# Kernel tuning notes

Hardware: AMD Instinct MI355X
Metric: run time of the kernel (lower is better)

## Reference

```python
import jax, jax.numpy as jnp
import numpy as np

ALPHA = 1.702
LIMIT = 7.0


def setup_inputs() -> dict:
    E, H, D = 16, 2880, 2880
    B, S = 2, 1024
    T = B * S
    key = jax.random.key(0)
    ks = jax.random.split(key, 8)
    hidden_states = jax.random.normal(ks[0], (B, S, H), dtype=jnp.float32)
    routing_weights = jax.random.uniform(ks[1], (T, E), dtype=jnp.float32)
    scale = 0.02
    Wg = jax.random.normal(ks[2], (E, H, D), dtype=jnp.float32) * scale
    bg = jax.random.normal(ks[3], (E, D), dtype=jnp.float32) * scale
    Wu = jax.random.normal(ks[4], (E, H, D), dtype=jnp.float32) * scale
    bu = jax.random.normal(ks[5], (E, D), dtype=jnp.float32) * scale
    Wd = jax.random.normal(ks[6], (E, D, H), dtype=jnp.float32) * scale
    bd = jax.random.normal(ks[7], (E, H), dtype=jnp.float32) * scale
    return {"hidden_states": hidden_states, "routing_weights": routing_weights,
            "Wg": Wg, "bg": bg, "Wu": Wu, "bu": bu, "Wd": Wd, "bd": bd}


def reference(hidden_states, routing_weights, Wg, bg, Wu, bu, Wd, bd):
    orig_shape = hidden_states.shape
    H = Wg.shape[1]
    x = hidden_states.reshape(-1, H)  # [T, H]
    # per-expert gate/up projections: [E, T, D]
    gate = jnp.einsum('th,ehd->etd', x, Wg) + bg[:, None, :]
    gate = jnp.minimum(gate, LIMIT)
    up = jnp.einsum('th,ehd->etd', x, Wu) + bu[:, None, :]
    up = jnp.clip(up, -LIMIT, LIMIT)
    glu = gate * jax.nn.sigmoid(gate * ALPHA)
    inter = (up + 1.0) * glu  # [E, T, D]
    # down projection: [E, T, H]
    down = jnp.einsum('etd,edh->eth', inter, Wd) + bd[:, None, :]
    # routing-weighted sum over experts: [T, H]
    out = jnp.einsum('eth,te->th', down, routing_weights)
    return out.reshape(orig_shape)
```

## Files before the change

### kernel.cpp

```cpp
#include <hip/hip_runtime.h>
#include <cstdint>


#define ALPHA 1.702f
#define LIMIT 7.0f

static constexpr int E = 16;
static constexpr int H = 2880;
static constexpr int D = 2880;
static constexpr int T = 2048;
static constexpr int NKT = 45;
static constexpr int NG  = 4;
static constexpr int DP  = 3072;
static constexpr int NPR = 2*DP;

typedef float        f32x4  __attribute__((ext_vector_type(4)));
typedef short        bf16x8 __attribute__((ext_vector_type(8)));

#define MFMA_BF16(a,b,c) __builtin_amdgcn_mfma_f32_16x16x32_bf16((a),(b),(c),0,0,0)
#define SBAR()        __builtin_amdgcn_s_barrier()
#define SCHED_FENCE() __builtin_amdgcn_sched_barrier(0)
#define PRIO1()       __builtin_amdgcn_s_setprio(1)
#define PRIO0()       __builtin_amdgcn_s_setprio(0)
#define LGK0()        asm volatile("s_waitcnt lgkmcnt(0)" ::: "memory")
#define VMC6()        asm volatile("s_waitcnt vmcnt(6)" ::: "memory")

__device__ __forceinline__ unsigned short f2bf(float f){
  unsigned u = __builtin_bit_cast(unsigned, f);
  u += 0x7fffu + ((u >> 16) & 1u);
  return (unsigned short)(u >> 16);
}
__device__ __forceinline__ unsigned pack2(float a, float b){
  return (unsigned)f2bf(a) | ((unsigned)f2bf(b) << 16);
}

__device__ __forceinline__ void gload_lds16(const void* g, void* l){
  __builtin_amdgcn_global_load_lds((const __attribute__((address_space(1))) unsigned*)g,
                                   (__attribute__((address_space(3))) unsigned*)l,
                                   16, 0, 0);
}

__global__ void cvt_kernel(const float* __restrict__ in, unsigned short* __restrict__ ob, int n8){
  int i = blockIdx.x * 256 + threadIdx.x;
  if (i < n8){
    float4 a = ((const float4*)in)[2*i];
    float4 b = ((const float4*)in)[2*i+1];
    uint4 o;
    o.x = pack2(a.x, a.y); o.y = pack2(a.z, a.w);
    o.z = pack2(b.x, b.y); o.w = pack2(b.z, b.w);
    ((uint4*)ob)[i] = o;
  }
}

__global__ __launch_bounds__(256) void tcvt_kernel(
    const float* __restrict__ src, unsigned short* __restrict__ dst,
    int mode, size_t dstStride)
{
  __shared__ unsigned short tl[64*72];
  const int t = threadIdx.x;
  const float* s = src + (size_t)blockIdx.z * H * D;
  unsigned short* o = dst + (size_t)blockIdx.z * dstStride;
  const int r0 = blockIdx.x * 64, c0 = blockIdx.y * 64;

  if (c0 < D){
    int rr = t >> 2;
    #pragma unroll
    for (int p = 0; p < 4; ++p){
      int cc = ((t & 3) + p*4) * 4;
      float4 v = *(const float4*)(s + (size_t)(r0 + rr)*D + c0 + cc);
      tl[(cc+0)*72 + rr] = f2bf(v.x);
      tl[(cc+1)*72 + rr] = f2bf(v.y);
      tl[(cc+2)*72 + rr] = f2bf(v.z);
      tl[(cc+3)*72 + rr] = f2bf(v.w);
    }
    __syncthreads();
    #pragma unroll
    for (int p = 0; p < 2; ++p){
      int task = p*256 + t;
      int cl = task >> 3, ch = task & 7;
      int c = c0 + cl;
      int rowp = (mode < 2) ? ((c >> 5)*64 + (c & 31) + mode*32) : c;
      bf16x8 v = *(const bf16x8*)&tl[cl*72 + ch*8];
      *(bf16x8*)(o + (size_t)rowp*H + r0 + ch*8) = v;
    }
  } else {
    #pragma unroll
    for (int p = 0; p < 2; ++p){
      int task = p*256 + t;
      int cl = task >> 3, ch = task & 7;
      int c = c0 + cl;
      int rowp = (c >> 5)*64 + (c & 31) + mode*32;
      bf16x8 z = (bf16x8){0,0,0,0,0,0,0,0};
      *(bf16x8*)(o + (size_t)rowp*H + r0 + ch*8) = z;
    }
  }
}

__global__ void reduce_kernel(const float* __restrict__ p, float* __restrict__ out, int n4){
  int i = blockIdx.x * 256 + threadIdx.x;
  if (i < n4){
    f32x4 a = ((const f32x4*)p)[i];
    #pragma unroll
    for (int g = 1; g < NG; ++g)
      a += ((const f32x4*)(p + (size_t)g * T * H))[i];
    ((f32x4*)out)[i] = a;
  }
}

__global__ __launch_bounds__(512, 2) void gateup_kernel(
    const unsigned short* __restrict__ xb,
    const unsigned short* __restrict__ wGU,
    const float* __restrict__ bg,
    const float* __restrict__ bu,
    unsigned short* __restrict__ inter,
    int e0)
{
  __shared__ short As[2][256*64];
  __shared__ short Bs[2][256*64];

  const int t = threadIdx.x, lane = t & 63, wv = t >> 6;
  const int wm = wv >> 2, wn = wv & 3;

  int nbx = gridDim.x, nby = gridDim.y;
  int lin = blockIdx.x + nbx*(blockIdx.y + nby*blockIdx.z);
  int per = (nbx*nby*gridDim.z) >> 3;
  int id2 = (lin & 7)*per + (lin >> 3);
  int bx = id2 % nbx; int rem = id2 / nbx;
  int by = rem % nby; int ez = rem / nby;

  const int trow0 = bx*256, ncol0 = by*256;
  const int e = e0 + ez;
  const unsigned short* wg = wGU + (size_t)ez * NPR * H;

  f32x4 acc[8][4];
  #pragma unroll
  for (int i = 0; i < 8; ++i)
    #pragma unroll
    for (int j = 0; j < 4; ++j) acc[i][j] = (f32x4){0.f,0.f,0.f,0.f};

  auto stageA = [&](int kt, int b, int h){
    #pragma unroll
    for (int r2 = 0; r2 < 2; ++r2){
      int task = r2*512 + t;
      int ps = task >> 3, ch = task & 7, sch = ch ^ (ps & 7);
      int lr = h*64 + (ps & 63) + ((ps >> 6) << 7);
      gload_lds16(xb + (size_t)(trow0 + lr)*H + kt*64 + sch*8,
                  &As[b][h*8192 + task*8]);
    }
  };
  auto stageB = [&](int kt, int b, int h){
    #pragma unroll
    for (int r2 = 0; r2 < 2; ++r2){
      int task = r2*512 + t;
      int ps = task >> 3, ch = task & 7, sch = ch ^ (ps & 7);
      int lr = h*32 + ((ps >> 5) << 6) + (ps & 31);
      gload_lds16(wg + (size_t)(ncol0 + lr)*H + kt*64 + sch*8,
                  &Bs[b][h*8192 + task*8]);
    }
  };

  bf16x8 af[4][2], bLo[2][2], bHi[2][2];
  auto readAh = [&](int b, int qa){
    #pragma unroll
    for (int mi = 0; mi < 4; ++mi){
      int r = wm*128 + qa*64 + mi*16 + (lane & 15);
      int q = r >> 6, qs = ((q & 1) << 1) | (q >> 1);
      int pr = qs*64 + (r & 63);
      #pragma unroll
      for (int kk = 0; kk < 2; ++kk){
        int pc = (kk*4 + (lane >> 4)) ^ (pr & 7);
        af[mi][kk] = *(const bf16x8*)&As[b][pr*64 + pc*8];
      }
    }
  };
  auto readBh = [&](bf16x8 (&bf)[2][2], int b, int hb){
    #pragma unroll
    for (int ni = 0; ni < 2; ++ni){
      int rB = wn*64 + hb*32 + ni*16 + (lane & 15);
      int pr = ((rB >> 5) & 1)*128 + (rB >> 6)*32 + (rB & 31);
      #pragma unroll
      for (int kk = 0; kk < 2; ++kk){
        int pc = (kk*4 + (lane >> 4)) ^ (pr & 7);
        bf[ni][kk] = *(const bf16x8*)&Bs[b][pr*64 + pc*8];
      }
    }
  };
  auto mfmaQ = [&](bf16x8 (&bf)[2][2], int qa, int hb){
    #pragma unroll
    for (int kk = 0; kk < 2; ++kk)
      #pragma unroll
      for (int ni = 0; ni < 2; ++ni)
        #pragma unroll
        for (int mi = 0; mi < 4; ++mi)
          acc[qa*4+mi][hb*2+ni] = MFMA_BF16(af[mi][kk], bf[ni][kk], acc[qa*4+mi][hb*2+ni]);
  };

  stageA(0,0,0); stageB(0,0,0); stageB(0,0,1); stageA(0,0,1);
  stageA(1,1,0); stageB(1,1,0); stageB(1,1,1);
  asm volatile("s_waitcnt vmcnt(8)" ::: "memory");
  SBAR();

  for (int it = 0; it < 22; ++it){
    int kt = 2*it;
    int ktA = (kt+2 < NKT) ? kt+2 : NKT-1;
    int ktB = (kt+3 < NKT) ? kt+3 : NKT-1;
    readAh(0, 0); readBh(bLo, 0, 0);
    stageA(kt+1, 1, 1);
    SCHED_FENCE(); SBAR(); LGK0(); SCHED_FENCE();
    PRIO1(); mfmaQ(bLo, 0, 0); PRIO0();
    VMC6(); SBAR();
    readBh(bHi, 0, 1);
    stageA(ktA, 0, 0);
    SCHED_FENCE(); SBAR(); LGK0(); SCHED_FENCE();
    PRIO1(); mfmaQ(bHi, 0, 1); PRIO0();
    VMC6(); SBAR();
    readAh(0, 1);
    stageB(ktA, 0, 0);
    SCHED_FENCE(); SBAR(); LGK0(); SCHED_FENCE();
    PRIO1(); mfmaQ(bHi, 1, 1); PRIO0();
    VMC6(); SBAR();
    stageB(ktA, 0, 1);
    SCHED_FENCE(); SBAR(); SCHED_FENCE();
    PRIO1(); mfmaQ(bLo, 1, 0); PRIO0();
    VMC6(); SBAR();
    readAh(1, 0); readBh(bLo, 1, 0);
    stageA(ktA, 0, 1);
    SCHED_FENCE(); SBAR(); LGK0(); SCHED_FENCE();
    PRIO1(); mfmaQ(bLo, 0, 0); PRIO0();
    VMC6(); SBAR();
    readBh(bHi, 1, 1);
    stageA(ktB, 1, 0);
    SCHED_FENCE(); SBAR(); LGK0(); SCHED_FENCE();
    PRIO1(); mfmaQ(bHi, 0, 1); PRIO0();
    VMC6(); SBAR();
    readAh(1, 1);
    stageB(ktB, 1, 0);
    SCHED_FENCE(); SBAR(); LGK0(); SCHED_FENCE();
    PRIO1(); mfmaQ(bHi, 1, 1); PRIO0();
    VMC6(); SBAR();
    stageB(ktB, 1, 1);
    SCHED_FENCE(); SBAR(); SCHED_FENCE();
    PRIO1(); mfmaQ(bLo, 1, 0); PRIO0();
    VMC6(); SBAR();
  }

  asm volatile("s_waitcnt vmcnt(0)" ::: "memory");
  SBAR();
  readAh(0, 0); readBh(bLo, 0, 0); readBh(bHi, 0, 1);
  LGK0(); SCHED_FENCE();
  mfmaQ(bLo, 0, 0); mfmaQ(bHi, 0, 1);
  readAh(0, 1);
  LGK0(); SCHED_FENCE();
  mfmaQ(bHi, 1, 1); mfmaQ(bLo, 1, 0);

  const float* bgp = bg + (size_t)e * D;
  const float* bup = bu + (size_t)e * D;
  unsigned short* ip = inter + (size_t)ez * T * D;
  const int dbase = (by*4 + wn) * 32;
  #pragma unroll
  for (int g = 0; g < 2; ++g){
    int d0 = dbase + g*16;
    if (d0 < D){
      int d = d0 + (lane & 15);
      float bgv = bgp[d], buv = bup[d];
      #pragma unroll
      for (int mi = 0; mi < 8; ++mi){
        #pragma unroll
        for (int r = 0; r < 4; ++r){
          int trw = trow0 + wm*128 + mi*16 + (lane >> 4)*4 + r;
          float gv = acc[mi][g][r] + bgv;
          float uv = acc[mi][g+2][r] + buv;
          gv = fminf(gv, LIMIT);
          uv = fminf(fmaxf(uv, -LIMIT), LIMIT);
          float glu = gv / (1.f + __expf(-ALPHA * gv));
          ip[(size_t)trw * D + d] = f2bf((uv + 1.f) * glu);
        }
      }
    }
  }
}

__global__ __launch_bounds__(256, 2) void down_kernel(
    const unsigned short* __restrict__ inter,
    const unsigned short* __restrict__ wdT,
    const float* __restrict__ bd,
    const float* __restrict__ rw,
    float* __restrict__ pout,
    int e0, int ec)
{
  __shared__ short As[2][128*64];
  __shared__ short Bs[2][192*64];

  const int t = threadIdx.x, lane = t & 63, wv = t >> 6;
  const int wm = wv >> 1, wn = wv & 1;

  int nbx = gridDim.x, nby = gridDim.y;
  int lin = blockIdx.x + nbx*(blockIdx.y + nby*blockIdx.z);
  int per = (nbx*nby*gridDim.z) >> 3;
  int id2 = (lin & 7)*per + (lin >> 3);
  int bx = id2 % nbx; int rem = id2 / nbx;
  int by = rem % nby; int g  = rem / nby;

  const int trow0 = bx * 128, ncol0 = by * 192;
  const int ne = (ec > g) ? ((ec - 1 - g) >> 2) + 1 : 0;

  f32x4 oacc[4][6];
  #pragma unroll
  for (int i = 0; i < 4; ++i)
    #pragma unroll
    for (int j = 0; j < 6; ++j) oacc[i][j] = (f32x4){0.f,0.f,0.f,0.f};

  auto stage = [&](int ee, int kt, int buf){
    const unsigned short* ap = inter + (size_t)ee * T * D;
    const unsigned short* wd = wdT + (size_t)ee * H * D;
    #pragma unroll
    for (int i = 0; i < 4; ++i){
      int task = i*256 + t, row = task >> 3, ch = task & 7, sch = ch ^ (row & 7);
      gload_lds16(ap + (size_t)(trow0 + row)*D + kt*64 + sch*8, &As[buf][task*8]);
    }
    #pragma unroll
    for (int j = 0; j < 6; ++j){
      int task = j*256 + t, row = task >> 3, ch = task & 7, sch = ch ^ (row & 7);
      gload_lds16(wd + (size_t)(ncol0 + row)*D + kt*64 + sch*8, &Bs[buf][task*8]);
    }
  };

  if (ne > 0){
    stage(g, 0, 0);

    int gkt = 0;
    for (int ei = 0; ei < ne; ++ei){
      const int ee = g + ei*4;
      const int e  = e0 + ee;
      f32x4 acc[4][6];
      #pragma unroll
      for (int i = 0; i < 4; ++i)
        #pragma unroll
        for (int j = 0; j < 6; ++j) acc[i][j] = (f32x4){0.f,0.f,0.f,0.f};

      for (int kt = 0; kt < NKT; ++kt, ++gkt){
        int cur = gkt & 1, nxt = cur ^ 1;
        int eeN, ktN;
        if (kt+1 < NKT)      { eeN = ee;     ktN = kt+1; }
        else if (ei+1 < ne)  { eeN = ee + 4; ktN = 0;    }
        else                 { eeN = ee;     ktN = kt;   }
        stage(eeN, ktN, nxt);
        asm volatile("s_waitcnt vmcnt(10)" ::: "memory");
        SCHED_FENCE(); SBAR(); SCHED_FENCE();
        #pragma unroll
        for (int kk = 0; kk < 2; ++kk){
          bf16x8 af2[4];
          #pragma unroll
          for (int mi = 0; mi < 4; ++mi){
            int row = wm*64 + mi*16 + (lane & 15);
            int pc  = (kk*4 + (lane>>4)) ^ (row & 7);
            af2[mi] = *(const bf16x8*)&As[cur][row*64 + pc*8];
          }
          bf16x8 fb[6];
          #pragma unroll
          for (int ni = 0; ni < 6; ++ni){
            int row = wn*96 + ni*16 + (lane & 15);
            int pc  = (kk*4 + (lane>>4)) ^ (row & 7);
            fb[ni] = *(const bf16x8*)&Bs[cur][row*64 + pc*8];
          }
          #pragma unroll
          for (int ni = 0; ni < 6; ++ni)
            #pragma unroll
            for (int mi = 0; mi < 4; ++mi)
              acc[mi][ni] = MFMA_BF16(af2[mi], fb[ni], acc[mi][ni]);
        }
        SBAR();
      }

      const float* bdp = bd + (size_t)e * H;
      #pragma unroll
      for (int ni = 0; ni < 6; ++ni){
        int h = ncol0 + wn*96 + ni*16 + (lane & 15);
        float bdv = bdp[h];
        #pragma unroll
        for (int mi = 0; mi < 4; ++mi){
          #pragma unroll
          for (int r = 0; r < 4; ++r){
            int trw = trow0 + wm*64 + mi*16 + (lane >> 4)*4 + r;
            float rv = rw[trw*E + e];
            oacc[mi][ni][r] += rv * (acc[mi][ni][r] + bdv);
          }
        }
      }
    }
    asm volatile("s_waitcnt vmcnt(0)" ::: "memory");
  }

  float* pp = pout + (size_t)g * T * H;
  const int accum = (e0 != 0);
  #pragma unroll
  for (int ni = 0; ni < 6; ++ni){
    int h = ncol0 + wn*96 + ni*16 + (lane & 15);
    #pragma unroll
    for (int mi = 0; mi < 4; ++mi){
      #pragma unroll
      for (int r = 0; r < 4; ++r){
        int trw = trow0 + wm*64 + mi*16 + (lane >> 4)*4 + r;
        size_t oi = (size_t)trw * H + h;
        float v = oacc[mi][ni][r];
        if (accum) v += pp[oi];
        pp[oi] = v;
      }
    }
  }
}

extern "C" void kernel_launch(void* const* d_in, const int* in_sizes, int n_in,
                              void* d_out, int out_size, void* d_ws, size_t ws_size,
                              hipStream_t stream) {
  const float* hs  = (const float*)d_in[0];
  const float* rwt = (const float*)d_in[1];
  const float* Wg  = (const float*)d_in[2];
  const float* bg  = (const float*)d_in[3];
  const float* Wu  = (const float*)d_in[4];
  const float* bu  = (const float*)d_in[5];
  const float* Wd  = (const float*)d_in[6];
  const float* bd  = (const float*)d_in[7];
  float* out = (float*)d_out;

  const size_t xbytes = (size_t)T * H * 2;
  const size_t poutB  = (size_t)NG * T * H * 4;
  const size_t interB = (size_t)T * D * 2;
  const size_t guB    = (size_t)NPR * H * 2;
  const size_t perE   = interB + guB;

  long long avail = (long long)ws_size - (long long)(xbytes + poutB);
  int EC = (int)(avail / (long long)perE);
  if (EC < 1) EC = 1;
  if (EC > E) EC = E;

  unsigned short* xb    = (unsigned short*)d_ws;
  float*          pout  = (float*)((char*)d_ws + xbytes);
  unsigned short* inter = (unsigned short*)((char*)d_ws + xbytes + poutB);
  unsigned short* wGU   = (unsigned short*)((char*)d_ws + xbytes + poutB + (size_t)EC*interB);
  unsigned short* wdT   = wGU;

  cvt_kernel<<<(T*H/8 + 255)/256, 256, 0, stream>>>(hs, xb, T*H/8);

  for (int e0 = 0; e0 < E; e0 += EC){
    int ec = (E - e0 < EC) ? (E - e0) : EC;
    tcvt_kernel<<<dim3(45,48,ec), 256, 0, stream>>>(Wg + (size_t)e0*H*D, wGU, 0, (size_t)NPR*H);
    tcvt_kernel<<<dim3(45,48,ec), 256, 0, stream>>>(Wu + (size_t)e0*H*D, wGU, 1, (size_t)NPR*H);
    gateup_kernel<<<dim3(8, 24, ec), 512, 0, stream>>>(xb, wGU, bg, bu, inter, e0);
    tcvt_kernel<<<dim3(45,45,ec), 256, 0, stream>>>(Wd + (size_t)e0*D*H, wdT, 2, (size_t)D*H);
    down_kernel<<<dim3(16, 15, NG), 256, 0, stream>>>(inter, wdT, bd, rwt, pout, e0, ec);
  }
  reduce_kernel<<<(T*H/4 + 255)/256, 256, 0, stream>>>(pout, out, T*H/4);
}
```

Baseline: 2.175 ms.

## Overlap next chunk's weight transpose-convert with current down-projection GEMM

The next expert chunk's Wg/Wu/Wd fp32→bf16 transpose-conversion now runs as extra blocks appended to the down_kernel grid. Memory-bound conversion work can then run concurrently with the down GEMM instead of as separate serialized launches. The transposed Wd buffer is double-buffered and the chunk size is capped at 8 experts so the pipeline has at least two stages. The cost is long-running converter blocks in the grid, which may create tail imbalance or compete with the GEMM blocks for bandwidth and CUs.

```diff
diff --git a/kernel.cpp b/kernel.cpp
--- a/kernel.cpp
+++ b/kernel.cpp
@@ -13,6 +13,7 @@
 static constexpr int NG  = 4;
 static constexpr int DP  = 3072;
 static constexpr int NPR = 2*DP;
+static constexpr int NBGEMM = 16*15*NG;
 
 typedef float        f32x4  __attribute__((ext_vector_type(4)));
 typedef short        bf16x8 __attribute__((ext_vector_type(8)));
@@ -128,9 +129,10 @@
   int bx = id2 % nbx; int rem = id2 / nbx;
   int by = rem % nby; int ez = rem / nby;
 
-  const int trow0 = bx*256, ncol0 = by*256;
+  const int trow0 = bx*256;
   const int e = e0 + ez;
   const unsigned short* wg = wGU + (size_t)ez * NPR * H;
+  const int ncol0 = by*256;
 
   f32x4 acc[8][4];
   #pragma unroll
@@ -286,20 +288,76 @@
     const float* __restrict__ bd,
     const float* __restrict__ rw,
     float* __restrict__ pout,
-    int e0, int ec)
+    int e0, int ec,
+    const float* __restrict__ Wg, const float* __restrict__ Wu,
+    const float* __restrict__ Wd,
+    unsigned short* __restrict__ wGUn,
+    unsigned short* __restrict__ wdTn,
+    int e0N, int ecN)
 {
-  __shared__ short As[2][128*64];
-  __shared__ short Bs[2][192*64];
-
-  const int t = threadIdx.x, lane = t & 63, wv = t >> 6;
+  __shared__ __attribute__((aligned(16))) unsigned char ldsb[81920];
+  auto As = (short(*)[128*64])(ldsb);
+  auto Bs = (short(*)[192*64])(ldsb + 32768);
+  unsigned short* tl = (unsigned short*)ldsb;
+
+  const int t = threadIdx.x;
+  const int flat = blockIdx.x;
+
+  if (flat >= NBGEMM){
+    int sid = flat - NBGEMM;
+    int perm = 45 * ecN;
+    int mat = sid / perm, rem2 = sid % perm;
+    int ez = rem2 / 45, cs = rem2 % 45;
+    const float* src; unsigned short* dst; int mode;
+    if (mat == 0){ src = Wg + (size_t)(e0N+ez)*H*D; dst = wGUn + (size_t)ez*NPR*H; mode = 0; }
+    else if (mat == 1){ src = Wu + (size_t)(e0N+ez)*H*D; dst = wGUn + (size_t)ez*NPR*H; mode = 1; }
+    else { src = Wd + (size_t)(e0N+ez)*H*D; dst = wdTn + (size_t)ez*D*H; mode = 2; }
+    const int c0 = cs*64;
+    const int rr = t >> 2;
+    float4 pv[4];
+    auto ld = [&](int r0){
+      #pragma unroll
+      for (int p = 0; p < 4; ++p){
+        int cc = ((t & 3) + p*4) * 4;
+        pv[p] = *(const float4*)(src + (size_t)(r0 + rr)*D + c0 + cc);
+      }
+    };
+    ld(0);
+    for (int r0 = 0; r0 < H; r0 += 64){
+      float4 cv[4];
+      #pragma unroll
+      for (int p = 0; p < 4; ++p) cv[p] = pv[p];
+      if (r0 + 64 < H) ld(r0 + 64);
+      #pragma unroll
+      for (int p = 0; p < 4; ++p){
+        int cc = ((t & 3) + p*4) * 4;
+        tl[(cc+0)*72 + rr] = f2bf(cv[p].x);
+        tl[(cc+1)*72 + rr] = f2bf(cv[p].y);
+        tl[(cc+2)*72 + rr] = f2bf(cv[p].z);
+        tl[(cc+3)*72 + rr] = f2bf(cv[p].w);
+      }
+      __syncthreads();
+      #pragma unroll
+      for (int p = 0; p < 2; ++p){
+        int task = p*256 + t;
+        int cl = task >> 3, ch = task & 7;
+        int c = c0 + cl;
+        int rowp = (mode < 2) ? ((c >> 5)*64 + (c & 31) + mode*32) : c;
+        bf16x8 v = *(const bf16x8*)&tl[cl*72 + ch*8];
+        *(bf16x8*)(dst + (size_t)rowp*H + r0 + ch*8) = v;
+      }
+      __syncthreads();
+    }
+    return;
+  }
+
+  const int lane = t & 63, wv = t >> 6;
   const int wm = wv >> 1, wn = wv & 1;
 
-  int nbx = gridDim.x, nby = gridDim.y;
-  int lin = blockIdx.x + nbx*(blockIdx.y + nby*blockIdx.z);
-  int per = (nbx*nby*gridDim.z) >> 3;
-  int id2 = (lin & 7)*per + (lin >> 3);
-  int bx = id2 % nbx; int rem = id2 / nbx;
-  int by = rem % nby; int g  = rem / nby;
+  int perb = NBGEMM >> 3;
+  int id2 = (flat & 7)*perb + (flat >> 3);
+  int bx = id2 % 16; int rem = id2 / 16;
+  int by = rem % 15; int g = rem / 15;
 
   const int trow0 = bx * 128, ncol0 = by * 192;
   const int ne = (ec > g) ? ((ec - 1 - g) >> 2) + 1 : 0;
@@ -427,28 +485,41 @@
   const size_t poutB  = (size_t)NG * T * H * 4;
   const size_t interB = (size_t)T * D * 2;
   const size_t guB    = (size_t)NPR * H * 2;
-  const size_t perE   = interB + guB;
+  const size_t wdB    = (size_t)D * H * 2;
+  const size_t perE   = interB + guB + 2*wdB;
 
   long long avail = (long long)ws_size - (long long)(xbytes + poutB);
   int EC = (int)(avail / (long long)perE);
   if (EC < 1) EC = 1;
-  if (EC > E) EC = E;
+  if (EC > 8) EC = 8;
 
   unsigned short* xb    = (unsigned short*)d_ws;
   float*          pout  = (float*)((char*)d_ws + xbytes);
   unsigned short* inter = (unsigned short*)((char*)d_ws + xbytes + poutB);
-  unsigned short* wGU   = (unsigned short*)((char*)d_ws + xbytes + poutB + (size_t)EC*interB);
-  unsigned short* wdT   = wGU;
+  unsigned short* wGU   = inter + (size_t)EC * T * D;
+  unsigned short* wdT0  = wGU + (size_t)EC * NPR * H;
+  unsigned short* wdT1  = wdT0 + (size_t)EC * D * H;
+
+  int e0s[16], ecs[16], nch = 0;
+  for (int e0 = 0; e0 < E; e0 += EC){ e0s[nch] = e0; ecs[nch] = (E-e0 < EC)?(E-e0):EC; ++nch; }
 
   cvt_kernel<<<(T*H/8 + 255)/256, 256, 0, stream>>>(hs, xb, T*H/8);
 
-  for (int e0 = 0; e0 < E; e0 += EC){
-    int ec = (E - e0 < EC) ? (E - e0) : EC;
-    tcvt_kernel<<<dim3(45,48,ec), 256, 0, stream>>>(Wg + (size_t)e0*H*D, wGU, 0, (size_t)NPR*H);
-    tcvt_kernel<<<dim3(45,48,ec), 256, 0, stream>>>(Wu + (size_t)e0*H*D, wGU, 1, (size_t)NPR*H);
-    gateup_kernel<<<dim3(8, 24, ec), 512, 0, stream>>>(xb, wGU, bg, bu, inter, e0);
-    tcvt_kernel<<<dim3(45,45,ec), 256, 0, stream>>>(Wd + (size_t)e0*D*H, wdT, 2, (size_t)D*H);
-    down_kernel<<<dim3(16, 15, NG), 256, 0, stream>>>(inter, wdT, bd, rwt, pout, e0, ec);
+  tcvt_kernel<<<dim3(45,48,ecs[0]), 256, 0, stream>>>(Wg + (size_t)e0s[0]*H*D, wGU, 0, (size_t)NPR*H);
+  tcvt_kernel<<<dim3(45,48,ecs[0]), 256, 0, stream>>>(Wu + (size_t)e0s[0]*H*D, wGU, 1, (size_t)NPR*H);
+  tcvt_kernel<<<dim3(45,45,ecs[0]), 256, 0, stream>>>(Wd + (size_t)e0s[0]*H*D, wdT0, 2, (size_t)D*H);
+
+  for (int i = 0; i < nch; ++i){
+    unsigned short* wdCur = (i & 1) ? wdT1 : wdT0;
+    unsigned short* wdNxt = (i & 1) ? wdT0 : wdT1;
+    gateup_kernel<<<dim3(8, 24, ecs[i]), 512, 0, stream>>>(xb, wGU, bg, bu, inter, e0s[i]);
+    int e0N = (i+1 < nch) ? e0s[i+1] : 0;
+    int ecN = (i+1 < nch) ? ecs[i+1] : 0;
+    int nstr = 3 * 45 * ecN;
+    down_kernel<<<dim3(NBGEMM + nstr), 256, 0, stream>>>(
+        inter, wdCur, bd, rwt, pout, e0s[i], ecs[i],
+        Wg + (size_t)e0N*H*D, Wu + (size_t)e0N*H*D, Wd + (size_t)e0N*H*D,
+        wGU, wdNxt, 0, ecN);
   }
   reduce_kernel<<<(T*H/4 + 255)/256, 256, 0, stream>>>(pout, out, T*H/4);
 }
```

Measured after the change: 2.151 ms. About the same (-1.1%).

## Fold routing weight into inter and restructure down GEMM per expert

Applied to the files above, without the earlier changes.

The routing weight is now multiplied into the intermediate activations inside the gate/up epilogue, so the down projection becomes a plain per-expert GEMM. The down kernel is rebuilt to match the 256x256, 512-thread gate/up schedule: ping-pong quarter tiles with staged loads and priority hints, one expert per grid z, padded Wd layout, and its own workspace buffers instead of sharing with the gate/up weights. Partial outputs are kept per expert and summed by the reduce kernel. This raises parallelism and MFMA efficiency in the down GEMM, but costs more workspace and more reduce traffic over EC slices. Rounding the scaled activations to bf16 before the down projection slightly changes numerics.

```diff
diff --git a/kernel.cpp b/kernel.cpp
--- a/kernel.cpp
+++ b/kernel.cpp
@@ -10,7 +10,6 @@
 static constexpr int D = 2880;
 static constexpr int T = 2048;
 static constexpr int NKT = 45;
-static constexpr int NG  = 4;
 static constexpr int DP  = 3072;
 static constexpr int NPR = 2*DP;
 
@@ -89,19 +88,19 @@
       int task = p*256 + t;
       int cl = task >> 3, ch = task & 7;
       int c = c0 + cl;
-      int rowp = (c >> 5)*64 + (c & 31) + mode*32;
+      int rowp = (mode < 2) ? ((c >> 5)*64 + (c & 31) + mode*32) : c;
       bf16x8 z = (bf16x8){0,0,0,0,0,0,0,0};
       *(bf16x8*)(o + (size_t)rowp*H + r0 + ch*8) = z;
     }
   }
 }
 
-__global__ void reduce_kernel(const float* __restrict__ p, float* __restrict__ out, int n4){
+__global__ void reduce_kernel(const float* __restrict__ p, float* __restrict__ out,
+                              int n4, int nz){
   int i = blockIdx.x * 256 + threadIdx.x;
   if (i < n4){
     f32x4 a = ((const f32x4*)p)[i];
-    #pragma unroll
-    for (int g = 1; g < NG; ++g)
+    for (int g = 1; g < nz; ++g)
       a += ((const f32x4*)(p + (size_t)g * T * H))[i];
     ((f32x4*)out)[i] = a;
   }
@@ -112,6 +111,7 @@
     const unsigned short* __restrict__ wGU,
     const float* __restrict__ bg,
     const float* __restrict__ bu,
+    const float* __restrict__ rw,
     unsigned short* __restrict__ inter,
     int e0)
 {
@@ -273,138 +273,181 @@
           gv = fminf(gv, LIMIT);
           uv = fminf(fmaxf(uv, -LIMIT), LIMIT);
           float glu = gv / (1.f + __expf(-ALPHA * gv));
-          ip[(size_t)trw * D + d] = f2bf((uv + 1.f) * glu);
+          float rv = rw[trw*E + e];
+          ip[(size_t)trw * D + d] = f2bf(rv * (uv + 1.f) * glu);
         }
       }
     }
   }
 }
 
-__global__ __launch_bounds__(256, 2) void down_kernel(
+__global__ __launch_bounds__(512, 2) void down_kernel(
     const unsigned short* __restrict__ inter,
     const unsigned short* __restrict__ wdT,
     const float* __restrict__ bd,
     const float* __restrict__ rw,
     float* __restrict__ pout,
-    int e0, int ec)
+    int e0)
 {
-  __shared__ short As[2][128*64];
-  __shared__ short Bs[2][192*64];
+  __shared__ short As[2][256*64];
+  __shared__ short Bs[2][256*64];
 
   const int t = threadIdx.x, lane = t & 63, wv = t >> 6;
-  const int wm = wv >> 1, wn = wv & 1;
+  const int wm = wv >> 2, wn = wv & 3;
 
   int nbx = gridDim.x, nby = gridDim.y;
   int lin = blockIdx.x + nbx*(blockIdx.y + nby*blockIdx.z);
   int per = (nbx*nby*gridDim.z) >> 3;
   int id2 = (lin & 7)*per + (lin >> 3);
   int bx = id2 % nbx; int rem = id2 / nbx;
-  int by = rem % nby; int g  = rem / nby;
-
-  const int trow0 = bx * 128, ncol0 = by * 192;
-  const int ne = (ec > g) ? ((ec - 1 - g) >> 2) + 1 : 0;
-
-  f32x4 oacc[4][6];
+  int by = rem % nby; int ez = rem / nby;
+
+  const int trow0 = bx*256, ncol0 = by*256;
+  const int e = e0 + ez;
+  const unsigned short* ap = inter + (size_t)ez * T * D;
+  const unsigned short* wd = wdT + (size_t)ez * DP * D;
+
+  f32x4 acc[8][4];
   #pragma unroll
-  for (int i = 0; i < 4; ++i)
-    #pragma unroll
-    for (int j = 0; j < 6; ++j) oacc[i][j] = (f32x4){0.f,0.f,0.f,0.f};
-
-  auto stage = [&](int ee, int kt, int buf){
-    const unsigned short* ap = inter + (size_t)ee * T * D;
-    const unsigned short* wd = wdT + (size_t)ee * H * D;
-    #pragma unroll
-    for (int i = 0; i < 4; ++i){
-      int task = i*256 + t, row = task >> 3, ch = task & 7, sch = ch ^ (row & 7);
-      gload_lds16(ap + (size_t)(trow0 + row)*D + kt*64 + sch*8, &As[buf][task*8]);
-    }
-    #pragma unroll
-    for (int j = 0; j < 6; ++j){
-      int task = j*256 + t, row = task >> 3, ch = task & 7, sch = ch ^ (row & 7);
-      gload_lds16(wd + (size_t)(ncol0 + row)*D + kt*64 + sch*8, &Bs[buf][task*8]);
-    }
-  };
-
-  if (ne > 0){
-    stage(g, 0, 0);
-
-    int gkt = 0;
-    for (int ei = 0; ei < ne; ++ei){
-      const int ee = g + ei*4;
-      const int e  = e0 + ee;
-      f32x4 acc[4][6];
-      #pragma unroll
-      for (int i = 0; i < 4; ++i)
+  for (int i = 0; i < 8; ++i)
+    #pragma unroll
+    for (int j = 0; j < 4; ++j) acc[i][j] = (f32x4){0.f,0.f,0.f,0.f};
+
+  auto stageA = [&](int kt, int b, int h){
+    #pragma unroll
+    for (int r2 = 0; r2 < 2; ++r2){
+      int task = r2*512 + t;
+      int ps = task >> 3, ch = task & 7, sch = ch ^ (ps & 7);
+      int lr = h*64 + (ps & 63) + ((ps >> 6) << 7);
+      gload_lds16(ap + (size_t)(trow0 + lr)*D + kt*64 + sch*8,
+                  &As[b][h*8192 + task*8]);
+    }
+  };
+  auto stageB = [&](int kt, int b, int h){
+    #pragma unroll
+    for (int r2 = 0; r2 < 2; ++r2){
+      int task = r2*512 + t;
+      int ps = task >> 3, ch = task & 7, sch = ch ^ (ps & 7);
+      int lr = h*32 + ((ps >> 5) << 6) + (ps & 31);
+      gload_lds16(wd + (size_t)(ncol0 + lr)*D + kt*64 + sch*8,
+                  &Bs[b][h*8192 + task*8]);
+    }
+  };
+
+  bf16x8 af[4][2], bLo[2][2], bHi[2][2];
+  auto readAh = [&](int b, int qa){
+    #pragma unroll
+    for (int mi = 0; mi < 4; ++mi){
+      int r = wm*128 + qa*64 + mi*16 + (lane & 15);
+      int q = r >> 6, qs = ((q & 1) << 1) | (q >> 1);
+      int pr = qs*64 + (r & 63);
+      #pragma unroll
+      for (int kk = 0; kk < 2; ++kk){
+        int pc = (kk*4 + (lane >> 4)) ^ (pr & 7);
+        af[mi][kk] = *(const bf16x8*)&As[b][pr*64 + pc*8];
+      }
+    }
+  };
+  auto readBh = [&](bf16x8 (&bf)[2][2], int b, int hb){
+    #pragma unroll
+    for (int ni = 0; ni < 2; ++ni){
+      int rB = wn*64 + hb*32 + ni*16 + (lane & 15);
+      int pr = ((rB >> 5) & 1)*128 + (rB >> 6)*32 + (rB & 31);
+      #pragma unroll
+      for (int kk = 0; kk < 2; ++kk){
+        int pc = (kk*4 + (lane >> 4)) ^ (pr & 7);
+        bf[ni][kk] = *(const bf16x8*)&Bs[b][pr*64 + pc*8];
+      }
+    }
+  };
+  auto mfmaQ = [&](bf16x8 (&bf)[2][2], int qa, int hb){
+    #pragma unroll
+    for (int kk = 0; kk < 2; ++kk)
+      #pragma unroll
+      for (int ni = 0; ni < 2; ++ni)
         #pragma unroll
-        for (int j = 0; j < 6; ++j) acc[i][j] = (f32x4){0.f,0.f,0.f,0.f};
-
-      for (int kt = 0; kt < NKT; ++kt, ++gkt){
-        int cur = gkt & 1, nxt = cur ^ 1;
-        int eeN, ktN;
-        if (kt+1 < NKT)      { eeN = ee;     ktN = kt+1; }
-        else if (ei+1 < ne)  { eeN = ee + 4; ktN = 0;    }
-        else                 { eeN = ee;     ktN = kt;   }
-        stage(eeN, ktN, nxt);
-        asm volatile("s_waitcnt vmcnt(10)" ::: "memory");
-        SCHED_FENCE(); SBAR(); SCHED_FENCE();
-        #pragma unroll
-        for (int kk = 0; kk < 2; ++kk){
-          bf16x8 af2[4];
-          #pragma unroll
-          for (int mi = 0; mi < 4; ++mi){
-            int row = wm*64 + mi*16 + (lane & 15);
-            int pc  = (kk*4 + (lane>>4)) ^ (row & 7);
-            af2[mi] = *(const bf16x8*)&As[cur][row*64 + pc*8];
-          }
-          bf16x8 fb[6];
-          #pragma unroll
-          for (int ni = 0; ni < 6; ++ni){
-            int row = wn*96 + ni*16 + (lane & 15);
-            int pc  = (kk*4 + (lane>>4)) ^ (row & 7);
-            fb[ni] = *(const bf16x8*)&Bs[cur][row*64 + pc*8];
-          }
-          #pragma unroll
-          for (int ni = 0; ni < 6; ++ni)
-            #pragma unroll
-            for (int mi = 0; mi < 4; ++mi)
-              acc[mi][ni] = MFMA_BF16(af2[mi], fb[ni], acc[mi][ni]);
-        }
-        SBAR();
-      }
-
-      const float* bdp = bd + (size_t)e * H;
-      #pragma unroll
-      for (int ni = 0; ni < 6; ++ni){
-        int h = ncol0 + wn*96 + ni*16 + (lane & 15);
-        float bdv = bdp[h];
-        #pragma unroll
-        for (int mi = 0; mi < 4; ++mi){
-          #pragma unroll
-          for (int r = 0; r < 4; ++r){
-            int trw = trow0 + wm*64 + mi*16 + (lane >> 4)*4 + r;
-            float rv = rw[trw*E + e];
-            oacc[mi][ni][r] += rv * (acc[mi][ni][r] + bdv);
-          }
-        }
-      }
-    }
-    asm volatile("s_waitcnt vmcnt(0)" ::: "memory");
-  }
-
-  float* pp = pout + (size_t)g * T * H;
+        for (int mi = 0; mi < 4; ++mi)
+          acc[qa*4+mi][hb*2+ni] = MFMA_BF16(af[mi][kk], bf[ni][kk], acc[qa*4+mi][hb*2+ni]);
+  };
+
+  stageA(0,0,0); stageB(0,0,0); stageB(0,0,1); stageA(0,0,1);
+  stageA(1,1,0); stageB(1,1,0); stageB(1,1,1);
+  asm volatile("s_waitcnt vmcnt(8)" ::: "memory");
+  SBAR();
+
+  for (int it = 0; it < 22; ++it){
+    int kt = 2*it;
+    int ktA = (kt+2 < NKT) ? kt+2 : NKT-1;
+    int ktB = (kt+3 < NKT) ? kt+3 : NKT-1;
+    readAh(0, 0); readBh(bLo, 0, 0);
+    stageA(kt+1, 1, 1);
+    SCHED_FENCE(); SBAR(); LGK0(); SCHED_FENCE();
+    PRIO1(); mfmaQ(bLo, 0, 0); PRIO0();
+    VMC6(); SBAR();
+    readBh(bHi, 0, 1);
+    stageA(ktA, 0, 0);
+    SCHED_FENCE(); SBAR(); LGK0(); SCHED_FENCE();
+    PRIO1(); mfmaQ(bHi, 0, 1); PRIO0();
+    VMC6(); SBAR();
+    readAh(0, 1);
+    stageB(ktA, 0, 0);
+    SCHED_FENCE(); SBAR(); LGK0(); SCHED_FENCE();
+    PRIO1(); mfmaQ(bHi, 1, 1); PRIO0();
+    VMC6(); SBAR();
+    stageB(ktA, 0, 1);
+    SCHED_FENCE(); SBAR(); SCHED_FENCE();
+    PRIO1(); mfmaQ(bLo, 1, 0); PRIO0();
+    VMC6(); SBAR();
+    readAh(1, 0); readBh(bLo, 1, 0);
+    stageA(ktA, 0, 1);
+    SCHED_FENCE(); SBAR(); LGK0(); SCHED_FENCE();
+    PRIO1(); mfmaQ(bLo, 0, 0); PRIO0();
+    VMC6(); SBAR();
+    readBh(bHi, 1, 1);
+    stageA(ktB, 1, 0);
+    SCHED_FENCE(); SBAR(); LGK0(); SCHED_FENCE();
+    PRIO1(); mfmaQ(bHi, 0, 1); PRIO0();
+    VMC6(); SBAR();
+    readAh(1, 1);
+    stageB(ktB, 1, 0);
+    SCHED_FENCE(); SBAR(); LGK0(); SCHED_FENCE();
+    PRIO1(); mfmaQ(bHi, 1, 1); PRIO0();
+    VMC6(); SBAR();
+    stageB(ktB, 1, 1);
+    SCHED_FENCE(); SBAR(); SCHED_FENCE();
+    PRIO1(); mfmaQ(bLo, 1, 0); PRIO0();
+    VMC6(); SBAR();
+  }
+
+  asm volatile("s_waitcnt vmcnt(0)" ::: "memory");
+  SBAR();
+  readAh(0, 0); readBh(bLo, 0, 0); readBh(bHi, 0, 1);
+  LGK0(); SCHED_FENCE();
+  mfmaQ(bLo, 0, 0); mfmaQ(bHi, 0, 1);
+  readAh(0, 1);
+  LGK0(); SCHED_FENCE();
+  mfmaQ(bHi, 1, 1); mfmaQ(bLo, 1, 0);
+
+  const float* bdp = bd + (size_t)e * H;
+  float* pp = pout + (size_t)ez * T * H;
   const int accum = (e0 != 0);
   #pragma unroll
-  for (int ni = 0; ni < 6; ++ni){
-    int h = ncol0 + wn*96 + ni*16 + (lane & 15);
-    #pragma unroll
-    for (int mi = 0; mi < 4; ++mi){
-      #pragma unroll
-      for (int r = 0; r < 4; ++r){
-        int trw = trow0 + wm*64 + mi*16 + (lane >> 4)*4 + r;
-        size_t oi = (size_t)trw * H + h;
-        float v = oacc[mi][ni][r];
-        if (accum) v += pp[oi];
-        pp[oi] = v;
+  for (int j = 0; j < 4; ++j){
+    int h0 = ncol0 + wn*64 + j*16;
+    if (h0 < H){
+      int h = h0 + (lane & 15);
+      float bdv = bdp[h];
+      #pragma unroll
+      for (int mi = 0; mi < 8; ++mi){
+        #pragma unroll
+        for (int r = 0; r < 4; ++r){
+          int trw = trow0 + wm*128 + mi*16 + (lane >> 4)*4 + r;
+          float rv = rw[trw*E + e];
+          size_t oi = (size_t)trw * H + h;
+          float v = acc[mi][j][r] + rv * bdv;
+          if (accum) v += pp[oi];
+          pp[oi] = v;
+        }
       }
     }
   }
@@ -424,21 +467,22 @@
   float* out = (float*)d_out;
 
   const size_t xbytes = (size_t)T * H * 2;
-  const size_t poutB  = (size_t)NG * T * H * 4;
   const size_t interB = (size_t)T * D * 2;
   const size_t guB    = (size_t)NPR * H * 2;
-  const size_t perE   = interB + guB;
-
-  long long avail = (long long)ws_size - (long long)(xbytes + poutB);
+  const size_t wdB    = (size_t)DP * D * 2;
+  const size_t poutE  = (size_t)T * H * 4;
+  const size_t perE   = interB + guB + wdB + poutE;
+
+  long long avail = (long long)ws_size - (long long)xbytes;
   int EC = (int)(avail / (long long)perE);
   if (EC < 1) EC = 1;
   if (EC > E) EC = E;
 
   unsigned short* xb    = (unsigned short*)d_ws;
   float*          pout  = (float*)((char*)d_ws + xbytes);
-  unsigned short* inter = (unsigned short*)((char*)d_ws + xbytes + poutB);
-  unsigned short* wGU   = (unsigned short*)((char*)d_ws + xbytes + poutB + (size_t)EC*interB);
-  unsigned short* wdT   = wGU;
+  unsigned short* inter = (unsigned short*)((char*)d_ws + xbytes + (size_t)EC*poutE);
+  unsigned short* wGU   = inter + (size_t)EC * T * D;
+  unsigned short* wdT   = wGU + (size_t)EC * NPR * H;
 
   cvt_kernel<<<(T*H/8 + 255)/256, 256, 0, stream>>>(hs, xb, T*H/8);
 
@@ -446,9 +490,9 @@
     int ec = (E - e0 < EC) ? (E - e0) : EC;
     tcvt_kernel<<<dim3(45,48,ec), 256, 0, stream>>>(Wg + (size_t)e0*H*D, wGU, 0, (size_t)NPR*H);
     tcvt_kernel<<<dim3(45,48,ec), 256, 0, stream>>>(Wu + (size_t)e0*H*D, wGU, 1, (size_t)NPR*H);
-    gateup_kernel<<<dim3(8, 24, ec), 512, 0, stream>>>(xb, wGU, bg, bu, inter, e0);
-    tcvt_kernel<<<dim3(45,45,ec), 256, 0, stream>>>(Wd + (size_t)e0*D*H, wdT, 2, (size_t)D*H);
-    down_kernel<<<dim3(16, 15, NG), 256, 0, stream>>>(inter, wdT, bd, rwt, pout, e0, ec);
-  }
-  reduce_kernel<<<(T*H/4 + 255)/256, 256, 0, stream>>>(pout, out, T*H/4);
-}
+    gateup_kernel<<<dim3(8, 24, ec), 512, 0, stream>>>(xb, wGU, bg, bu, rwt, inter, e0);
+    tcvt_kernel<<<dim3(45,48,ec), 256, 0, stream>>>(Wd + (size_t)e0*H*D, wdT, 2, (size_t)DP*D);
+    down_kernel<<<dim3(8, 12, ec), 512, 0, stream>>>(inter, wdT, bd, rwt, pout, e0);
+  }
+  reduce_kernel<<<(T*H/4 + 255)/256, 256, 0, stream>>>(pout, out, T*H/4, EC);
+}
```

Measured after the change: 2.134 ms. About the same (-1.9%).
